# Optimization experiments

Measured on AMD Instinct MI355X. Metric: run time of the kernel, lower is better.

Reference implementation:

```python
import jax, jax.numpy as jnp
import numpy as np

N = 102400      # total nodes
E = 1638400     # total edges (avg degree 16)
B = 2048        # number of graphs
DIN = 128       # input feature dim
K = 30          # sort-pool k


def setup_inputs() -> dict:
    key = jax.random.key(0)
    ks = jax.random.split(key, 16)
    x = jax.random.normal(ks[0], (N, DIN), dtype=jnp.float32)
    edge_index = jax.random.randint(ks[1], (2, E), 0, N)
    batch = jnp.sort(jax.random.randint(ks[2], (N,), 0, B))

    def w(k, sh):
        return jax.random.normal(k, sh, dtype=jnp.float32) * 0.1

    return {
        "x": x, "edge_index": edge_index, "batch": batch,
        "W1": w(ks[3], (DIN, 32)), "b1": w(ks[4], (32,)),
        "W2": w(ks[5], (32, 32)), "b2": w(ks[6], (32,)),
        "W3": w(ks[7], (32, 32)), "b3": w(ks[8], (32,)),
        "W4": w(ks[9], (32, 1)), "b4": w(ks[10], (1,)),
        "conv1_w": w(ks[11], (16, 1, 97)), "conv1_b": w(ks[11], (16,)),
        "conv2_w": w(ks[12], (32, 16, 5)), "conv2_b": w(ks[12], (32,)),
        "lin1_w": w(ks[13], (352, 128)), "lin1_b": w(ks[13], (128,)),
        "lin2_w": w(ks[14], (128, 1)), "lin2_b": w(ks[14], (1,)),
    }


def _gcn(x, W, b, src, dst, dinv, n):
    # PyG GCNConv: D^{-1/2}(A+I)D^{-1/2} X W + b, transform first (small out dim)
    h = x @ W
    msg = h[src] * (dinv[src] * dinv[dst])[:, None]            # [E, F]
    agg = jax.ops.segment_sum(msg, dst, num_segments=n)        # neighbor aggregation
    agg = agg + h * (dinv * dinv)[:, None]                     # self-loop term (norm = 1/deg)
    return agg + b


def _sort_pool(h, batch, num_graphs, k):
    # global_sort_pool: per-graph descending sort by last channel, keep top-k, zero-pad
    n, f = h.shape
    order = jnp.lexsort((-h[:, -1], batch))                    # primary: graph id, secondary: -key
    hs, bs = h[order], batch[order]
    counts = jax.ops.segment_sum(jnp.ones(n, jnp.int32), batch, num_segments=num_graphs)
    starts = jnp.cumsum(counts) - counts                       # exclusive prefix
    pos = jnp.arange(n) - starts[bs]                           # rank within graph
    keep = pos < k
    out = jnp.zeros((num_graphs, k, f), h.dtype)
    out = out.at[bs, jnp.clip(pos, 0, k - 1)].add(jnp.where(keep[:, None], hs, 0.0))
    return out.reshape(num_graphs, k * f)


def _conv1d(x, w, b, stride):
    y = jax.lax.conv_general_dilated(x, w, (stride,), 'VALID',
                                     dimension_numbers=('NCH', 'OIH', 'NCH'))
    return y + b[None, :, None]


def reference(x, edge_index, batch, W1, b1, W2, b2, W3, b3, W4, b4,
              conv1_w, conv1_b, conv2_w, conv2_b, lin1_w, lin1_b, lin2_w, lin2_b):
    n = x.shape[0]
    src, dst = edge_index[0], edge_index[1]
    deg = jax.ops.segment_sum(jnp.ones(src.shape[0], x.dtype), dst, num_segments=n) + 1.0
    dinv = jax.lax.rsqrt(deg)

    h1 = jnp.tanh(_gcn(x, W1, b1, src, dst, dinv, n))
    h2 = jnp.tanh(_gcn(h1, W2, b2, src, dst, dinv, n))
    h3 = jnp.tanh(_gcn(h2, W3, b3, src, dst, dinv, n))
    h4 = jnp.tanh(_gcn(h3, W4, b4, src, dst, dinv, n))
    h = jnp.concatenate([h1, h2, h3, h4], axis=-1)             # [N, 97]

    h = _sort_pool(h, batch, B, K)                             # [B, 2910]
    h = h[:, None, :]                                          # [B, 1, 2910]
    h = jax.nn.relu(_conv1d(h, conv1_w, conv1_b, 97))          # [B, 16, 30]
    bsz, c, l = h.shape
    h = h.reshape(bsz, c, l // 2, 2).max(axis=-1)              # maxpool(2,2) -> [B,16,15]
    h = jax.nn.relu(_conv1d(h, conv2_w, conv2_b, 1))           # [B, 32, 11]
    h = h.reshape(bsz, -1)                                     # [B, 352]
    h = jax.nn.relu(h @ lin1_w + lin1_b)
    # Dropout(0.5) is identity at inference
    return jax.nn.sigmoid(h @ lin2_w + lin2_b)                 # [B, 1]
```

## Files before the change

### kernel.cpp

```cpp
#include <hip/hip_runtime.h>
#include <math.h>

#define NN 102400
#define NE 1638400
#define NG 2048
#define KTOP 30
#define NBUCK 400
#define EPB 4096
#define NB1 400

__global__ __launch_bounds__(256) void fused_front_kernel(
    const int* __restrict__ dst, int* __restrict__ hist1,
    const float* __restrict__ x, const float* __restrict__ W1,
    float* __restrict__ htmp,
    const int* __restrict__ batch, int* __restrict__ starts) {
    __shared__ float Wsh[128 * 32];
    __shared__ float Xs[128 * 33];
    __shared__ int hsh[NBUCK];
    int bid = blockIdx.x;
    int tid = threadIdx.x;

    if (bid < NB1) {
        for (int q = tid; q < NBUCK; q += 256) hsh[q] = 0;
        __syncthreads();
        const int4* dp = (const int4*)(dst + bid * EPB);
        for (int i4 = tid; i4 < EPB / 4; i4 += 256) {
            int4 dd = dp[i4];
            atomicAdd(&hsh[dd.x >> 8], 1);
            atomicAdd(&hsh[dd.y >> 8], 1);
            atomicAdd(&hsh[dd.z >> 8], 1);
            atomicAdd(&hsh[dd.w >> 8], 1);
        }
        __syncthreads();
        for (int q = tid; q < NBUCK; q += 256) hist1[q * NB1 + bid] = hsh[q];
    } else if (bid < NB1 + 800) {
        int bidx = bid - NB1;
        int n_base = bidx * 128;
        for (int i = tid; i < 128 * 32; i += 256) Wsh[i] = W1[i];
        int jb = (tid >> 6) << 3;
        int q = tid & 63;
        float acc0[8], acc1[8];
#pragma unroll
        for (int j = 0; j < 8; ++j) { acc0[j] = 0.f; acc1[j] = 0.f; }
        for (int k0 = 0; k0 < 128; k0 += 32) {
            __syncthreads();
#pragma unroll
            for (int it = 0; it < 4; ++it) {
                int u = tid + 256 * it;
                int row = u >> 3;
                int c4 = u & 7;
                float4 v = *(const float4*)&x[(size_t)(n_base + row) * 128 + k0 + c4 * 4];
                *(float4*)&Xs[row * 33 + c4 * 4] = v;
            }
            __syncthreads();
#pragma unroll 8
            for (int kk = 0; kk < 32; ++kk) {
                float v0 = Xs[q * 33 + kk];
                float v1 = Xs[(q + 64) * 33 + kk];
                float4 wlo = *(const float4*)&Wsh[(k0 + kk) * 32 + jb];
                float4 whi = *(const float4*)&Wsh[(k0 + kk) * 32 + jb + 4];
                acc0[0] += v0 * wlo.x; acc0[1] += v0 * wlo.y;
                acc0[2] += v0 * wlo.z; acc0[3] += v0 * wlo.w;
                acc0[4] += v0 * whi.x; acc0[5] += v0 * whi.y;
                acc0[6] += v0 * whi.z; acc0[7] += v0 * whi.w;
                acc1[0] += v1 * wlo.x; acc1[1] += v1 * wlo.y;
                acc1[2] += v1 * wlo.z; acc1[3] += v1 * wlo.w;
                acc1[4] += v1 * whi.x; acc1[5] += v1 * whi.y;
                acc1[6] += v1 * whi.z; acc1[7] += v1 * whi.w;
            }
        }
        int n0 = n_base + q;
        int n1 = n0 + 64;
        float4 o0 = {acc0[0], acc0[1], acc0[2], acc0[3]};
        float4 o1 = {acc0[4], acc0[5], acc0[6], acc0[7]};
        float4 o2 = {acc1[0], acc1[1], acc1[2], acc1[3]};
        float4 o3 = {acc1[4], acc1[5], acc1[6], acc1[7]};
        *(float4*)&htmp[(size_t)n0 * 32 + jb] = o0;
        *(float4*)&htmp[(size_t)n0 * 32 + jb + 4] = o1;
        *(float4*)&htmp[(size_t)n1 * 32 + jb] = o2;
        *(float4*)&htmp[(size_t)n1 * 32 + jb + 4] = o3;
    } else {
        int i = (bid - NB1 - 800) * 256 + tid;
        if (i < NN) {
            int c = batch[i];
            int p = (i == 0) ? -1 : batch[i - 1];
            for (int g = p + 1; g <= c; ++g) starts[g] = i;
            if (i == NN - 1) {
                for (int g = c + 1; g <= NG; ++g) starts[g] = NN;
            }
        }
    }
}

__global__ __launch_bounds__(256) void s1a_kernel(const int* __restrict__ hist1,
                                                  int* __restrict__ offs,
                                                  int* __restrict__ totals) {
    __shared__ int A[512], B[512];
    int q = blockIdx.x, tid = threadIdx.x;
    int i0 = tid, i1 = tid + 256;
    int v0 = (i0 < NB1) ? hist1[q * NB1 + i0] : 0;
    int v1 = (i1 < NB1) ? hist1[q * NB1 + i1] : 0;
    A[i0] = v0; A[i1] = v1;
    __syncthreads();
    int* cur = A; int* nxt = B;
    for (int off = 1; off < 512; off <<= 1) {
        nxt[i0] = cur[i0] + ((i0 >= off) ? cur[i0 - off] : 0);
        nxt[i1] = cur[i1] + cur[i1 - off];
        __syncthreads();
        int* t = cur; cur = nxt; nxt = t;
    }
    if (i0 < NB1) offs[q * NB1 + i0] = cur[i0] - v0;
    if (i1 < NB1) offs[q * NB1 + i1] = cur[i1] - v1;
    if (tid == 0) totals[q] = cur[511];
}

__global__ __launch_bounds__(256) void s1b_kernel(const int* __restrict__ totals,
                                                  int* __restrict__ bucketStart,
                                                  int* __restrict__ rowptr) {
    __shared__ int A[512], B[512];
    int tid = threadIdx.x;
    int i0 = tid, i1 = tid + 256;
    int v0 = (i0 < NBUCK) ? totals[i0] : 0;
    int v1 = (i1 < NBUCK) ? totals[i1] : 0;
    A[i0] = v0; A[i1] = v1;
    __syncthreads();
    int* cur = A; int* nxt = B;
    for (int off = 1; off < 512; off <<= 1) {
        nxt[i0] = cur[i0] + ((i0 >= off) ? cur[i0 - off] : 0);
        nxt[i1] = cur[i1] + cur[i1 - off];
        __syncthreads();
        int* t = cur; cur = nxt; nxt = t;
    }
    if (i0 < NBUCK) bucketStart[i0] = cur[i0] - v0;
    if (i1 < NBUCK) bucketStart[i1] = cur[i1] - v1;
    if (tid == 0) { bucketStart[NBUCK] = cur[511]; rowptr[NN] = cur[511]; }
}

__global__ __launch_bounds__(256) void p1_kernel(const int* __restrict__ src,
                                                 const int* __restrict__ dst,
                                                 const int* __restrict__ offs,
                                                 const int* __restrict__ bucketStart,
                                                 unsigned int* __restrict__ ebuf) {
    __shared__ int myoff[NBUCK];
    int b = blockIdx.x, tid = threadIdx.x;
    for (int q = tid; q < NBUCK; q += 256)
        myoff[q] = bucketStart[q] + offs[q * NB1 + b];
    __syncthreads();
    const int4* dp = (const int4*)(dst + b * EPB);
    const int4* sp = (const int4*)(src + b * EPB);
    for (int i4 = tid; i4 < EPB / 4; i4 += 256) {
        int4 dd = dp[i4];
        int4 ss = sp[i4];
        int p0 = atomicAdd(&myoff[dd.x >> 8], 1);
        int p1 = atomicAdd(&myoff[dd.y >> 8], 1);
        int p2 = atomicAdd(&myoff[dd.z >> 8], 1);
        int p3 = atomicAdd(&myoff[dd.w >> 8], 1);
        ebuf[p0] = ((unsigned int)(dd.x & 255) << 24) | (unsigned int)ss.x;
        ebuf[p1] = ((unsigned int)(dd.y & 255) << 24) | (unsigned int)ss.y;
        ebuf[p2] = ((unsigned int)(dd.z & 255) << 24) | (unsigned int)ss.z;
        ebuf[p3] = ((unsigned int)(dd.w & 255) << 24) | (unsigned int)ss.w;
    }
}

__global__ __launch_bounds__(256) void p2_kernel(const unsigned int* __restrict__ ebuf,
                                                 const int* __restrict__ bucketStart,
                                                 int* __restrict__ csr_src,
                                                 int* __restrict__ rowptr,
                                                 float* __restrict__ dinv) {
    __shared__ int fcnt[256];
    __shared__ int tmp[256];
    __shared__ int foff[256];
    int q = blockIdx.x, tid = threadIdx.x;
    int base = bucketStart[q];
    int ecnt = bucketStart[q + 1] - base;
    fcnt[tid] = 0;
    __syncthreads();
    for (int i = tid; i < ecnt; i += 256) {
        unsigned int e = ebuf[base + i];
        atomicAdd(&fcnt[e >> 24], 1);
    }
    __syncthreads();
    int c = fcnt[tid];
    int n = q * 256 + tid;
    dinv[n] = rsqrtf((float)c + 1.0f);
    tmp[tid] = c;
    __syncthreads();
    for (int off = 1; off < 256; off <<= 1) {
        int u = (tid >= off) ? tmp[tid - off] : 0;
        __syncthreads();
        tmp[tid] += u;
        __syncthreads();
    }
    int excl = base + tmp[tid] - c;
    rowptr[n] = excl;
    foff[tid] = excl;
    __syncthreads();
    for (int i = tid; i < ecnt; i += 256) {
        unsigned int e = ebuf[base + i];
        int pos = atomicAdd(&foff[e >> 24], 1);
        csr_src[pos] = (int)(e & 0xFFFFFF);
    }
}

template <int NEXT>
__global__ __launch_bounds__(256) void gcn_aggd_kernel(
    const int* __restrict__ rowptr, const int* __restrict__ csr_src,
    const float* __restrict__ htmp, const float* __restrict__ dinv,
    const float* __restrict__ b, const float* __restrict__ Wn,
    float* __restrict__ hout, float* __restrict__ htn) {
    __shared__ float Ws[32 * 32];
    __shared__ float Hs[32][36];
    int tid = threadIdx.x;
    if (NEXT == 32) {
        for (int i = tid; i < 1024; i += 256) Ws[i] = Wn[i];
    } else {
        if (tid < 32) Ws[tid] = Wn[tid];
    }
    int idx = blockIdx.x * 256 + tid;
    int n = idx >> 3, fg = (idx & 7) << 2;
    int beg = rowptr[n], end = rowptr[n + 1];
    float di = dinv[n];
    float4 acc = {0.f, 0.f, 0.f, 0.f};
    int i = beg;
    for (; i + 7 < end; i += 8) {
        int s[8];
#pragma unroll
        for (int k = 0; k < 8; ++k) s[k] = csr_src[i + k];
        float c[8];
#pragma unroll
        for (int k = 0; k < 8; ++k) c[k] = dinv[s[k]] * di;
        float4 v[8];
#pragma unroll
        for (int k = 0; k < 8; ++k) v[k] = *(const float4*)&htmp[(size_t)s[k] * 32 + fg];
#pragma unroll
        for (int k = 0; k < 8; ++k) {
            acc.x += v[k].x * c[k]; acc.y += v[k].y * c[k];
            acc.z += v[k].z * c[k]; acc.w += v[k].w * c[k];
        }
    }
    for (; i + 3 < end; i += 4) {
        int s0 = csr_src[i], s1 = csr_src[i + 1];
        int s2 = csr_src[i + 2], s3 = csr_src[i + 3];
        float c0 = dinv[s0] * di, c1 = dinv[s1] * di;
        float c2 = dinv[s2] * di, c3 = dinv[s3] * di;
        float4 v0 = *(const float4*)&htmp[(size_t)s0 * 32 + fg];
        float4 v1 = *(const float4*)&htmp[(size_t)s1 * 32 + fg];
        float4 v2 = *(const float4*)&htmp[(size_t)s2 * 32 + fg];
        float4 v3 = *(const float4*)&htmp[(size_t)s3 * 32 + fg];
        acc.x += v0.x * c0; acc.y += v0.y * c0; acc.z += v0.z * c0; acc.w += v0.w * c0;
        acc.x += v1.x * c1; acc.y += v1.y * c1; acc.z += v1.z * c1; acc.w += v1.w * c1;
        acc.x += v2.x * c2; acc.y += v2.y * c2; acc.z += v2.z * c2; acc.w += v2.w * c2;
        acc.x += v3.x * c3; acc.y += v3.y * c3; acc.z += v3.z * c3; acc.w += v3.w * c3;
    }
    for (; i < end; ++i) {
        int s = csr_src[i];
        float c = dinv[s] * di;
        float4 v = *(const float4*)&htmp[(size_t)s * 32 + fg];
        acc.x += v.x * c; acc.y += v.y * c; acc.z += v.z * c; acc.w += v.w * c;
    }
    float dd = di * di;
    float4 hs = *(const float4*)&htmp[(size_t)n * 32 + fg];
    float4 bb = *(const float4*)&b[fg];
    float4 o;
    o.x = tanhf(acc.x + hs.x * dd + bb.x);
    o.y = tanhf(acc.y + hs.y * dd + bb.y);
    o.z = tanhf(acc.z + hs.z * dd + bb.z);
    o.w = tanhf(acc.w + hs.w * dd + bb.w);
    *(float4*)&hout[(size_t)n * 32 + fg] = o;
    int nl = tid >> 3;
    *(float4*)&Hs[nl][fg] = o;
    __syncthreads();
    if (NEXT == 32) {
        int n2 = tid >> 3, j4 = (tid & 7) << 2;
        int gnode = blockIdx.x * 32 + n2;
        float4 r = {0.f, 0.f, 0.f, 0.f};
#pragma unroll
        for (int k = 0; k < 32; ++k) {
            float h = Hs[n2][k];
            float4 wv = *(const float4*)&Ws[k * 32 + j4];
            r.x += h * wv.x; r.y += h * wv.y; r.z += h * wv.z; r.w += h * wv.w;
        }
        *(float4*)&htn[(size_t)gnode * 32 + j4] = r;
    } else {
        if (tid < 32) {
            int gnode = blockIdx.x * 32 + tid;
            float s = 0.f;
#pragma unroll
            for (int k = 0; k < 32; ++k) s += Hs[tid][k] * Ws[k];
            htn[gnode] = s;
        }
    }
}

__global__ __launch_bounds__(256) void gcn_agg1_kernel(
    const int* __restrict__ rowptr, const int* __restrict__ csr_src,
    const float* __restrict__ htmp, const float* __restrict__ dinv,
    const float* __restrict__ b, float* __restrict__ hout) {
    int n = blockIdx.x * blockDim.x + threadIdx.x;
    if (n >= NN) return;
    int beg = rowptr[n], end = rowptr[n + 1];
    float di = dinv[n];
    float acc = 0.f;
    int i = beg;
    for (; i + 7 < end; i += 8) {
        int s[8];
#pragma unroll
        for (int k = 0; k < 8; ++k) s[k] = csr_src[i + k];
        float c[8], v[8];
#pragma unroll
        for (int k = 0; k < 8; ++k) c[k] = dinv[s[k]] * di;
#pragma unroll
        for (int k = 0; k < 8; ++k) v[k] = htmp[s[k]];
#pragma unroll
        for (int k = 0; k < 8; ++k) acc += v[k] * c[k];
    }
    for (; i < end; ++i) {
        int s = csr_src[i];
        acc += htmp[s] * (dinv[s] * di);
    }
    hout[n] = tanhf(acc + htmp[n] * di * di + b[0]);
}


#define PSTR 100

__global__ __launch_bounds__(256) void pool_cnn_kernel(
    const float* __restrict__ h1, const float* __restrict__ h2,
    const float* __restrict__ h3, const float* __restrict__ h4,
    const int* __restrict__ starts,
    const float* __restrict__ c1w, const float* __restrict__ c1b,
    const float* __restrict__ c2w, const float* __restrict__ c2b,
    const float* __restrict__ l1w, const float* __restrict__ l1b,
    const float* __restrict__ l2w, const float* __restrict__ l2b,
    float* __restrict__ out) {
    __shared__ float P[KTOP][PSTR];
    __shared__ float CW[16 * PSTR];
    __shared__ float KY[480];
    float* keys = KY;
    float* y2  = &P[0][0];
    float* c2s = &P[0][0] + 240;
    float* y3  = KY;
    float* z   = KY + 352;
    int g = blockIdx.x;
    int tid = threadIdx.x;

    int start = starts[g];
    int end = starts[g + 1];
    int cnt = end - start;

    for (int i = tid; i < KTOP * PSTR; i += 256) (&P[0][0])[i] = 0.f;
    for (int i = tid; i < 16 * 97; i += 256) {
        int c = i / 97, f = i % 97;
        CW[c * PSTR + f] = c1w[i];
    }
    bool fits = (cnt <= 480);
    if (fits) {
        for (int i = tid; i < cnt; i += 256) keys[i] = h4[start + i];
    }
    __syncthreads();

    for (int i = tid; i < cnt; i += 256) {
        float key = fits ? keys[i] : h4[start + i];
        int rank = 0;
        if (fits) {
            for (int j = 0; j < cnt; ++j) {
                float kj = keys[j];
                rank += (kj > key) || (kj == key && j < i);
            }
        } else {
            for (int j = 0; j < cnt; ++j) {
                float kj = h4[start + j];
                rank += (kj > key) || (kj == key && j < i);
            }
        }
        if (rank < KTOP) {
            P[rank][96] = key;
            P[rank][97] = __int_as_float(start + i);
        }
    }
    __syncthreads();

    int nsel = (cnt < KTOP) ? cnt : KTOP;
    for (int u = tid; u < nsel * 24; u += 256) {
        int r = u / 24, q = u % 24;
        int node = __float_as_int(P[r][97]);
        const float* srcp = (q < 8) ? h1 : (q < 16) ? h2 : h3;
        int qq = q & 7;
        float4 v = *(const float4*)(srcp + (size_t)node * 32 + 4 * qq);
        *(float4*)&P[r][(q < 8 ? 0 : (q < 16 ? 32 : 64)) + 4 * qq] = v;
    }
    __syncthreads();

    if (tid < 120) {
        int t0 = tid >> 3;
        int c0 = tid & 7;
        const float* PrA = &P[t0][0];
        const float* PrB = &P[t0 + 15][0];
        const float* WrA = &CW[c0 * PSTR];
        const float* WrB = &CW[(c0 + 8) * PSTR];
        float bA = c1b[c0], bB = c1b[c0 + 8];
        float sAA = bA, sAB = bB, sBA = bA, sBB = bB;
#pragma unroll
        for (int f4 = 0; f4 < 24; ++f4) {
            float4 pA = *(const float4*)(PrA + 4 * f4);
            float4 pB = *(const float4*)(PrB + 4 * f4);
            float4 wA = *(const float4*)(WrA + 4 * f4);
            float4 wB = *(const float4*)(WrB + 4 * f4);
            sAA += wA.x * pA.x; sAA += wA.y * pA.y; sAA += wA.z * pA.z; sAA += wA.w * pA.w;
            sAB += wB.x * pA.x; sAB += wB.y * pA.y; sAB += wB.z * pA.z; sAB += wB.w * pA.w;
            sBA += wA.x * pB.x; sBA += wA.y * pB.y; sBA += wA.z * pB.z; sBA += wA.w * pB.w;
            sBB += wB.x * pB.x; sBB += wB.y * pB.y; sBB += wB.z * pB.z; sBB += wB.w * pB.w;
        }
        float kA = PrA[96], kB = PrB[96];
        sAA += WrA[96] * kA; sAB += WrB[96] * kA;
        sBA += WrA[96] * kB; sBB += WrB[96] * kB;
        KY[c0 * KTOP + t0]            = fmaxf(sAA, 0.f);
        KY[(c0 + 8) * KTOP + t0]      = fmaxf(sAB, 0.f);
        KY[c0 * KTOP + t0 + 15]       = fmaxf(sBA, 0.f);
        KY[(c0 + 8) * KTOP + t0 + 15] = fmaxf(sBB, 0.f);
    }
    __syncthreads();

    for (int o = tid; o < 16 * 15; o += 256) {
        int c = o / 15, t = o % 15;
        y2[o] = fmaxf(KY[c * KTOP + 2 * t], KY[c * KTOP + 2 * t + 1]);
    }
    for (int i = tid; i < 2560; i += 256) c2s[i] = c2w[i];
    __syncthreads();

    for (int o = tid; o < 32 * 11; o += 256) {
        int c = o / 11, t = o % 11;
        float s = c2b[c];
#pragma unroll
        for (int i = 0; i < 16; ++i)
#pragma unroll
            for (int j = 0; j < 5; ++j)
                s += c2s[(c * 16 + i) * 5 + j] * y2[i * 15 + t + j];
        y3[o] = fmaxf(s, 0.f);
    }
    __syncthreads();

    for (int o = tid; o < 128; o += 256) {
        float s = l1b[o];
#pragma unroll 16
        for (int i = 0; i < 352; ++i) s += y3[i] * l1w[i * 128 + o];
        z[o] = fmaxf(s, 0.f);
    }
    __syncthreads();

    if (tid == 0) {
        float s = l2b[0];
#pragma unroll 4
        for (int i = 0; i < 128; ++i) s += z[i] * l2w[i];
        out[g] = 1.f / (1.f + expf(-s));
    }
}

extern "C" void kernel_launch(void* const* d_in, const int* in_sizes, int n_in,
                              void* d_out, int out_size, void* d_ws, size_t ws_size,
                              hipStream_t stream) {
    const float* x   = (const float*)d_in[0];
    const int* ei    = (const int*)d_in[1];
    const int* batch = (const int*)d_in[2];
    const float* W1  = (const float*)d_in[3];
    const float* b1  = (const float*)d_in[4];
    const float* W2  = (const float*)d_in[5];
    const float* b2  = (const float*)d_in[6];
    const float* W3  = (const float*)d_in[7];
    const float* b3  = (const float*)d_in[8];
    const float* W4  = (const float*)d_in[9];
    const float* b4  = (const float*)d_in[10];
    const float* c1w = (const float*)d_in[11];
    const float* c1b = (const float*)d_in[12];
    const float* c2w = (const float*)d_in[13];
    const float* c2b = (const float*)d_in[14];
    const float* l1w = (const float*)d_in[15];
    const float* l1b = (const float*)d_in[16];
    const float* l2w = (const float*)d_in[17];
    const float* l2b = (const float*)d_in[18];
    float* out = (float*)d_out;

    const int* srcp = ei;
    const int* dstp = ei + NE;

    char* w = (char*)d_ws;
    float* dinv      = (float*)w;               w += sizeof(float) * NN;
    float* htmpA     = (float*)w;               w += sizeof(float) * NN * 32;
    float* htmpB     = (float*)w;               w += sizeof(float) * NN * 32;
    float* h1        = (float*)w;               w += sizeof(float) * NN * 32;
    float* h2        = (float*)w;               w += sizeof(float) * NN * 32;
    float* h3        = (float*)w;               w += sizeof(float) * NN * 32;
    float* h4        = (float*)w;               w += sizeof(float) * NN;
    int*   rowptr    = (int*)w;                 w += sizeof(int) * (NN + 1);
    int*   hist1     = (int*)w;                 w += sizeof(int) * NBUCK * NB1;
    int*   offs      = (int*)w;                 w += sizeof(int) * NBUCK * NB1;
    int*   totals    = (int*)w;                 w += sizeof(int) * NBUCK;
    int*   bucketStart = (int*)w;               w += sizeof(int) * (NBUCK + 1);
    int*   csr_src   = (int*)w;                 w += sizeof(int) * NE;
    int*   starts    = (int*)w;                 w += sizeof(int) * (NG + 1);

    unsigned int* ebuf = (unsigned int*)h2;

    fused_front_kernel<<<NB1 + 800 + 400, 256, 0, stream>>>(dstp, hist1, x, W1, htmpA,
                                                            batch, starts);
    s1a_kernel<<<NBUCK, 256, 0, stream>>>(hist1, offs, totals);
    s1b_kernel<<<1, 256, 0, stream>>>(totals, bucketStart, rowptr);
    p1_kernel<<<NB1, 256, 0, stream>>>(srcp, dstp, offs, bucketStart, ebuf);
    p2_kernel<<<NBUCK, 256, 0, stream>>>(ebuf, bucketStart, csr_src, rowptr, dinv);

    gcn_aggd_kernel<32><<<NN / 32, 256, 0, stream>>>(rowptr, csr_src, htmpA, dinv, b1,
                                                     W2, h1, htmpB);
    gcn_aggd_kernel<32><<<NN / 32, 256, 0, stream>>>(rowptr, csr_src, htmpB, dinv, b2,
                                                     W3, h2, htmpA);
    gcn_aggd_kernel<1><<<NN / 32, 256, 0, stream>>>(rowptr, csr_src, htmpA, dinv, b3,
                                                    W4, h3, htmpB);
    gcn_agg1_kernel<<<NN / 256, 256, 0, stream>>>(rowptr, csr_src, htmpB, dinv, b4, h4);

    pool_cnn_kernel<<<NG, 256, 0, stream>>>(h1, h2, h3, h4, starts,
                                            c1w, c1b, c2w, c2b,
                                            l1w, l1b, l2w, l2b, out);
}
```

Measured before the change: 221.4 us.

## Deepen gather unroll in GCN aggregation and register-block conv2 in pool kernel

Both the 32-feature and 1-feature GCN aggregation loops now unroll by 12 edges instead of 8 so more independent gathers are in flight. The single-feature kernel also gains a 4-edge tail loop. In the pool kernel, conv2 weights are stored with a padded stride of 81. Conv2 is now computed by 32 threads, one per output channel, each holding 11 accumulators and reusing y2 values from registers. This trades more register pressure and fewer active threads for lower shared-memory traffic and more memory-level parallelism.

After: 226.4 us. 1.02x slower.

```diff
diff --git a/kernel.cpp b/kernel.cpp
--- a/kernel.cpp
+++ b/kernel.cpp
@@ -222,18 +222,18 @@
     float di = dinv[n];
     float4 acc = {0.f, 0.f, 0.f, 0.f};
     int i = beg;
-    for (; i + 7 < end; i += 8) {
-        int s[8];
-#pragma unroll
-        for (int k = 0; k < 8; ++k) s[k] = csr_src[i + k];
-        float c[8];
-#pragma unroll
-        for (int k = 0; k < 8; ++k) c[k] = dinv[s[k]] * di;
-        float4 v[8];
-#pragma unroll
-        for (int k = 0; k < 8; ++k) v[k] = *(const float4*)&htmp[(size_t)s[k] * 32 + fg];
-#pragma unroll
-        for (int k = 0; k < 8; ++k) {
+    for (; i + 11 < end; i += 12) {
+        int s[12];
+#pragma unroll
+        for (int k = 0; k < 12; ++k) s[k] = csr_src[i + k];
+        float c[12];
+#pragma unroll
+        for (int k = 0; k < 12; ++k) c[k] = dinv[s[k]] * di;
+        float4 v[12];
+#pragma unroll
+        for (int k = 0; k < 12; ++k) v[k] = *(const float4*)&htmp[(size_t)s[k] * 32 + fg];
+#pragma unroll
+        for (int k = 0; k < 12; ++k) {
             acc.x += v[k].x * c[k]; acc.y += v[k].y * c[k];
             acc.z += v[k].z * c[k]; acc.w += v[k].w * c[k];
         }
@@ -302,17 +302,27 @@
     float di = dinv[n];
     float acc = 0.f;
     int i = beg;
-    for (; i + 7 < end; i += 8) {
-        int s[8];
-#pragma unroll
-        for (int k = 0; k < 8; ++k) s[k] = csr_src[i + k];
-        float c[8], v[8];
-#pragma unroll
-        for (int k = 0; k < 8; ++k) c[k] = dinv[s[k]] * di;
-#pragma unroll
-        for (int k = 0; k < 8; ++k) v[k] = htmp[s[k]];
-#pragma unroll
-        for (int k = 0; k < 8; ++k) acc += v[k] * c[k];
+    for (; i + 11 < end; i += 12) {
+        int s[12];
+#pragma unroll
+        for (int k = 0; k < 12; ++k) s[k] = csr_src[i + k];
+        float c[12], v[12];
+#pragma unroll
+        for (int k = 0; k < 12; ++k) c[k] = dinv[s[k]] * di;
+#pragma unroll
+        for (int k = 0; k < 12; ++k) v[k] = htmp[s[k]];
+#pragma unroll
+        for (int k = 0; k < 12; ++k) acc += v[k] * c[k];
+    }
+    for (; i + 3 < end; i += 4) {
+        int s0 = csr_src[i], s1 = csr_src[i + 1];
+        int s2 = csr_src[i + 2], s3 = csr_src[i + 3];
+        float c0 = dinv[s0] * di, c1 = dinv[s1] * di;
+        float c2 = dinv[s2] * di, c3 = dinv[s3] * di;
+        acc += htmp[s0] * c0;
+        acc += htmp[s1] * c1;
+        acc += htmp[s2] * c2;
+        acc += htmp[s3] * c3;
     }
     for (; i < end; ++i) {
         int s = csr_src[i];
@@ -323,6 +333,7 @@
 
 
 #define PSTR 100
+#define C2S 81
 
 __global__ __launch_bounds__(256) void pool_cnn_kernel(
     const float* __restrict__ h1, const float* __restrict__ h2,
@@ -425,18 +436,33 @@
         int c = o / 15, t = o % 15;
         y2[o] = fmaxf(KY[c * KTOP + 2 * t], KY[c * KTOP + 2 * t + 1]);
     }
-    for (int i = tid; i < 2560; i += 256) c2s[i] = c2w[i];
-    __syncthreads();
-
-    for (int o = tid; o < 32 * 11; o += 256) {
-        int c = o / 11, t = o % 11;
-        float s = c2b[c];
-#pragma unroll
-        for (int i = 0; i < 16; ++i)
-#pragma unroll
-            for (int j = 0; j < 5; ++j)
-                s += c2s[(c * 16 + i) * 5 + j] * y2[i * 15 + t + j];
-        y3[o] = fmaxf(s, 0.f);
+    for (int i = tid; i < 2560; i += 256) {
+        int c = i / 80, r = i % 80;
+        c2s[c * C2S + r] = c2w[i];
+    }
+    __syncthreads();
+
+    if (tid < 32) {
+        int c = tid;
+        float acc2[11];
+#pragma unroll
+        for (int t = 0; t < 11; ++t) acc2[t] = c2b[c];
+#pragma unroll
+        for (int i = 0; i < 16; ++i) {
+            float wv[5];
+#pragma unroll
+            for (int j = 0; j < 5; ++j) wv[j] = c2s[c * C2S + i * 5 + j];
+            float yv[15];
+#pragma unroll
+            for (int t = 0; t < 15; ++t) yv[t] = y2[i * 15 + t];
+#pragma unroll
+            for (int t = 0; t < 11; ++t) {
+#pragma unroll
+                for (int j = 0; j < 5; ++j) acc2[t] += wv[j] * yv[t + j];
+            }
+        }
+#pragma unroll
+        for (int t = 0; t < 11; ++t) y3[c * 11 + t] = fmaxf(acc2[t], 0.f);
     }
     __syncthreads();
 
```
